# Optimization experiments

Measured on AMD Instinct MI355X. Metric: run time of the kernel, lower is better.

Reference implementation:

```python
import jax, jax.numpy as jnp
import numpy as np

B, N, K, OUT = 8, 2048, 20, 40
BN_EPS = 1e-5  # torch BatchNorm default eps; inference with running_mean=0, running_var=1


def knn_idx(x, k):
    # x: (B, C, N). distance[b,n,m] = -||x_n||^2 - ||x_m||^2 + 2 x_n.x_m (negative sq dist)
    xsqu = jnp.sum(x * x, axis=1, keepdims=True)              # (B,1,N)
    xx = jnp.einsum('bcn,bcm->bnm', x, x)                     # (B,N,N)
    dist = 2.0 * xx - xsqu - jnp.transpose(xsqu, (0, 2, 1))   # (B,N,N)
    _, idx = jax.lax.top_k(dist, k)                           # (B,N,k) nearest (incl. self)
    return idx


def get_graph_feature(x, k):
    # x: (B, C, N) -> edge features (B, N, k, 2C) = concat(nbr - ctr, ctr)
    Bb = x.shape[0]
    idx = knn_idx(x, k)
    xt = jnp.transpose(x, (0, 2, 1))                          # (B,N,C)
    nbr = xt[jnp.arange(Bb)[:, None, None], idx]              # (B,N,k,C) gather
    ctr = xt[:, :, None, :]
    return jnp.concatenate([nbr - ctr, jnp.broadcast_to(ctr, nbr.shape)], axis=-1)


def bn(h, g, b):
    # inference BatchNorm with running_mean=0, running_var=1 (affine only)
    return h * (g / jnp.sqrt(1.0 + BN_EPS)) + b


def edge_conv(x, w, g, b, k):
    # EdgeConv: knn -> gather edge feats -> 1x1 conv -> BN -> ReLU -> max over k
    feat = get_graph_feature(x, k)                            # (B,N,k,2C)
    h = jnp.einsum('bnkc,oc->bnko', feat, w)                  # 1x1 conv
    h = jax.nn.relu(bn(h, g, b))
    h = jnp.max(h, axis=2)                                    # max pool over k -> (B,N,O)
    return jnp.transpose(h, (0, 2, 1))                        # (B,O,N)


def _forward(x, conv_w1, conv_w2, conv_w3, conv_w4, conv_w5, fc_w1, fc_w2, fc_w3,
             bn_g1, bn_b1, bn_g2, bn_b2, bn_g3, bn_b3, bn_g4, bn_b4,
             bn_g5, bn_b5, bn_g6, bn_b6, bn_g7, bn_b7, k):
    x1 = edge_conv(x, conv_w1, bn_g1, bn_b1, k)               # (B,64,N)
    x2 = edge_conv(x1, conv_w2, bn_g2, bn_b2, k)              # (B,64,N)
    x3 = edge_conv(x2, conv_w3, bn_g3, bn_b3, k)              # (B,128,N)
    x4 = edge_conv(x3, conv_w4, bn_g4, bn_b4, k)              # (B,256,N)
    xc = jnp.concatenate([x1, x2, x3, x4], axis=1)            # (B,512,N)
    h = jnp.einsum('bcn,oc->bon', xc, conv_w5)                # (B,1024,N)
    h = jax.nn.relu(bn(h, bn_g5[:, None], bn_b5[:, None]))
    h = jnp.max(h, axis=-1)                                   # global max pool -> (B,1024)
    h = jax.nn.relu(bn(h @ fc_w1.T, bn_g6, bn_b6))            # dropout = identity (eval)
    h = jax.nn.relu(bn(h @ fc_w2.T, bn_g7, bn_b7))
    return h @ fc_w3.T                                        # (B,OUT)


def setup_inputs() -> dict:
    key = jax.random.key(0)
    ks = jax.random.split(key, 32)
    def w(i, shape):
        return jax.random.normal(ks[i], shape, jnp.float32) / np.sqrt(shape[-1]).astype(np.float32)
    inp = {
        'x': jax.random.normal(ks[0], (B, 3, N), jnp.float32),
        'conv_w1': w(1, (64, 6)),
        'conv_w2': w(2, (64, 128)),
        'conv_w3': w(3, (128, 128)),
        'conv_w4': w(4, (256, 256)),
        'conv_w5': w(5, (1024, 512)),
        'fc_w1': w(6, (512, 1024)),
        'fc_w2': w(7, (256, 512)),
        'fc_w3': w(8, (OUT, 256)),
    }
    dims = [64, 64, 128, 256, 1024, 512, 256]
    for i, d in enumerate(dims):
        inp['bn_g%d' % (i + 1)] = jax.random.uniform(ks[9 + i], (d,), jnp.float32, 0.5, 1.5)
        inp['bn_b%d' % (i + 1)] = 0.05 * jax.random.normal(ks[16 + i], (d,), jnp.float32)
    inp['k'] = K
    return inp


def reference(x, conv_w1, conv_w2, conv_w3, conv_w4, conv_w5, fc_w1, fc_w2, fc_w3,
              bn_g1, bn_b1, bn_g2, bn_b2, bn_g3, bn_b3, bn_g4, bn_b4,
              bn_g5, bn_b5, bn_g6, bn_b6, bn_g7, bn_b7, k):
    return _forward(x, conv_w1, conv_w2, conv_w3, conv_w4, conv_w5, fc_w1, fc_w2, fc_w3,
                    bn_g1, bn_b1, bn_g2, bn_b2, bn_g3, bn_b3, bn_g4, bn_b4,
                    bn_g5, bn_b5, bn_g6, bn_b6, bn_g7, bn_b7, k)
```

## Files before the change

### kernel.cpp

```cpp
#include <hip/hip_runtime.h>
#include <hip/hip_bf16.h>
#include <math.h>

#define BATCH 8
#define NPTS  2048
#define KNN   20
#define NEG_INF (-3.402823466e38f)

static __device__ __forceinline__ float bn_scale(float g){ return g * rsqrtf(1.0f + 1e-5f); }

static __device__ __forceinline__ unsigned short bf16r(float f){
  unsigned int u = __float_as_uint(f);
  unsigned int r = (u + 0x7fffu + ((u >> 16) & 1u)) >> 16;
  return (unsigned short)r;
}
static __device__ __forceinline__ float bf2f(unsigned short h){
  return __uint_as_float((unsigned int)h << 16);
}
static __device__ __forceinline__ unsigned int fenc(float f){
  unsigned int u = __float_as_uint(f);
  return (u & 0x80000000u) ? ~u : (u | 0x80000000u);
}
static __device__ __forceinline__ float fdec(unsigned int e){
  return __uint_as_float((e & 0x80000000u) ? (e & 0x7fffffffu) : ~e);
}

using bfrag = __attribute__((ext_vector_type(8))) short;
using f32x4 = __attribute__((ext_vector_type(4))) float;

template<int CTRL>
static __device__ __forceinline__ void dpp_amax(float &bv, int &bi){
  int ov_i = __builtin_amdgcn_update_dpp(__float_as_int(NEG_INF), __float_as_int(bv),
                                         CTRL, 0xf, 0xf, false);
  int oi   = __builtin_amdgcn_update_dpp(0x7fffffff, bi, CTRL, 0xf, 0xf, false);
  float ov = __int_as_float(ov_i);
  if (ov > bv || (ov == bv && oi < bi)){ bv = ov; bi = oi; }
}
static __device__ __forceinline__ int wave_argmax_idx(float bv, int bi){
  dpp_amax<0x111>(bv, bi);
  dpp_amax<0x112>(bv, bi);
  dpp_amax<0x114>(bv, bi);
  dpp_amax<0x118>(bv, bi);
  dpp_amax<0x142>(bv, bi);
  dpp_amax<0x143>(bv, bi);
  return __builtin_amdgcn_readlane(bi, 63);
}
template<int CTRL>
static __device__ __forceinline__ float dpp_fadd(float v){
  int ov = __builtin_amdgcn_update_dpp(0, __float_as_int(v), CTRL, 0xf, 0xf, false);
  return v + __int_as_float(ov);
}
static __device__ __forceinline__ float wave_sum(float v){
  v = dpp_fadd<0x111>(v); v = dpp_fadd<0x112>(v);
  v = dpp_fadd<0x114>(v); v = dpp_fadd<0x118>(v);
  v = dpp_fadd<0x142>(v); v = dpp_fadd<0x143>(v);
  return __int_as_float(__builtin_amdgcn_readlane(__float_as_int(v), 63));
}

__global__ void sqnorm_kernel(const float* __restrict__ X, float* __restrict__ sq, int C){
  int i = blockIdx.x*blockDim.x + threadIdx.x;
  if (i >= BATCH*NPTS) return;
  int b = i / NPTS, n = i - b*NPTS;
  const float* xb = X + (size_t)b*C*NPTS + n;
  float s = 0.f;
  for (int c=0;c<C;++c){ float v = xb[(size_t)c*NPTS]; s += v*v; }
  sq[i] = s;
}

template<int C>
__global__ __launch_bounds__(256, 2) void knn_kernel(const float* __restrict__ X,
                                                     const float* __restrict__ sq,
                                                     int* __restrict__ idxout){
  const int b = blockIdx.y;
  const int n0 = blockIdx.x * 8;
  const int t = threadIdx.x;
  __shared__ __align__(16) float dist[4][NPTS];
  __shared__ float ctrs[C][8];
  __shared__ float sqn[8];
  const float* xb = X + (size_t)b*C*NPTS;
  for (int i=t; i<C*8; i+=256){
    int c = i >> 3, p = i & 7;
    ctrs[c][p] = xb[(size_t)c*NPTS + n0 + p];
  }
  if (t < 8) sqn[t] = sq[b*NPTS + n0 + t];
  __syncthreads();

  const int m0 = t * 8;
  float acc[8][8];
  #pragma unroll
  for (int i=0;i<8;++i)
    #pragma unroll
    for (int j=0;j<8;++j) acc[i][j] = 0.f;
  for (int c=0;c<C;++c){
    const float4 xa = *(const float4*)&xb[(size_t)c*NPTS + m0];
    const float4 xc = *(const float4*)&xb[(size_t)c*NPTS + m0 + 4];
    const float xm[8] = {xa.x,xa.y,xa.z,xa.w,xc.x,xc.y,xc.z,xc.w};
    #pragma unroll
    for (int i=0;i<8;++i){
      const float cv = ctrs[c][i];
      #pragma unroll
      for (int j=0;j<8;++j) acc[i][j] += cv*xm[j];
    }
  }
  {
    const float4 sa = *(const float4*)&sq[b*NPTS + m0];
    const float4 sb = *(const float4*)&sq[b*NPTS + m0 + 4];
    const float sm[8] = {sa.x,sa.y,sa.z,sa.w,sb.x,sb.y,sb.z,sb.w};
    #pragma unroll
    for (int i=0;i<8;++i){
      const float si = sqn[i];
      #pragma unroll
      for (int j=0;j<8;++j) acc[i][j] = 2.f*acc[i][j] - si - sm[j];
    }
  }

  const int wv = t >> 6, lane = t & 63;
  #pragma unroll
  for (int rep=0; rep<2; ++rep){
    #pragma unroll
    for (int i=0;i<4;++i){
      *(float4*)&dist[i][m0]   = make_float4(acc[rep*4+i][0],acc[rep*4+i][1],acc[rep*4+i][2],acc[rep*4+i][3]);
      *(float4*)&dist[i][m0+4] = make_float4(acc[rep*4+i][4],acc[rep*4+i][5],acc[rep*4+i][6],acc[rep*4+i][7]);
    }
    __syncthreads();
    float s0=NEG_INF,s1=NEG_INF,s2=NEG_INF,s3=NEG_INF;
    int   i0=0x7fffffff,i1=0x7fffffff,i2=0x7fffffff,i3=0x7fffffff;
    #pragma unroll
    for (int j=0;j<32;++j){
      const float v = dist[wv][lane + 64*j];
      const int   m = lane + 64*j;
      const bool b0 = v > s0, b1 = v > s1, b2 = v > s2, b3 = v > s3;
      const float n0 = b0 ? v : s0;            const int q0 = b0 ? m : i0;
      const float n1 = b0 ? s0 : (b1 ? v : s1); const int q1 = b0 ? i0 : (b1 ? m : i1);
      const float n2 = b1 ? s1 : (b2 ? v : s2); const int q2 = b1 ? i1 : (b2 ? m : i2);
      const float n3 = b2 ? s2 : (b3 ? v : s3); const int q3 = b2 ? i2 : (b3 ? m : i3);
      s0=n0;s1=n1;s2=n2;s3=n3; i0=q0;i1=q1;i2=q2;i3=q3;
    }
    int rem = 4;
    int* row = idxout + ((size_t)b*NPTS + n0 + rep*4 + wv)*KNN;
    for (int sel=0; sel<KNN; ++sel){
      const int widx = wave_argmax_idx(s0, i0);
      if (lane == 0) row[sel] = widx;
      if ((widx & 63) == lane){
        const float lastv = s0; const int lasti = i0;
        s0=s1;i0=i1; s1=s2;i1=i2; s2=s3;i2=i3;
        rem--;
        if (rem == 0){
          float nv = NEG_INF; int ni = 0x7fffffff;
          #pragma unroll
          for (int j=0;j<32;++j){
            const float vv = dist[wv][lane + 64*j];
            const int   mi = lane + 64*j;
            const bool ok = (vv < lastv) || (vv == lastv && mi > lasti);
            if (ok && vv > nv){ nv = vv; ni = mi; }
          }
          s0 = nv; i0 = ni; rem = 1;
        }
      }
    }
    __syncthreads();
  }
}

__global__ void wprep_kernel(const float* __restrict__ w, float* __restrict__ wnT,
                             float* __restrict__ wdT, int O, int C){
  int i = blockIdx.x*blockDim.x + threadIdx.x;
  if (i >= O*C) return;
  int c = i / O, o = i - c*O;
  float a = w[(size_t)o*2*C + c];
  wnT[(size_t)c*O + o] = a;
  wdT[(size_t)c*O + o] = w[(size_t)o*2*C + C + c] - a;
}

__global__ void wprep_bf_kernel(const float* __restrict__ w, unsigned short* __restrict__ wn,
                                unsigned short* __restrict__ wd, int O, int C){
  int i = blockIdx.x*blockDim.x + threadIdx.x;
  if (i >= O*C) return;
  int o = i / C, c = i - o*C;
  float a = w[(size_t)o*2*C + c];
  float d = w[(size_t)o*2*C + C + c] - a;
  wn[(size_t)o*C + c] = bf16r(a);
  wd[(size_t)o*C + c] = bf16r(d);
}

__global__ void bfsplit_kernel(const float* __restrict__ in, unsigned short* __restrict__ hi,
                               unsigned short* __restrict__ lo, int nq){
  int i = blockIdx.x*blockDim.x + threadIdx.x;
  if (i >= nq) return;
  float4 v = *(const float4*)&in[(size_t)i*4];
  unsigned short h0=bf16r(v.x), h1=bf16r(v.y), h2=bf16r(v.z), h3=bf16r(v.w);
  unsigned short l0=bf16r(v.x-bf2f(h0)), l1=bf16r(v.y-bf2f(h1)),
                 l2=bf16r(v.z-bf2f(h2)), l3=bf16r(v.w-bf2f(h3));
  *(uint2*)&hi[(size_t)i*4] = make_uint2((unsigned)h0|((unsigned)h1<<16), (unsigned)h2|((unsigned)h3<<16));
  *(uint2*)&lo[(size_t)i*4] = make_uint2((unsigned)l0|((unsigned)l1<<16), (unsigned)l2|((unsigned)l3<<16));
}

__global__ __launch_bounds__(256) void xcat_kernel(const float* __restrict__ x1T,
    const float* __restrict__ x2T, const float* __restrict__ x3T, const float* __restrict__ x4T,
    unsigned short* __restrict__ xhi, unsigned short* __restrict__ xlo){
  int i = blockIdx.x*blockDim.x + threadIdx.x;
  if (i >= BATCH*NPTS*128) return;
  int q = i & 127, bn_ = i >> 7;
  int k = q*4;
  const float* src; int kk;
  if (k < 64)      { src = x1T + (size_t)bn_*64;  kk = k; }
  else if (k <128) { src = x2T + (size_t)bn_*64;  kk = k-64; }
  else if (k <256) { src = x3T + (size_t)bn_*128; kk = k-128; }
  else             { src = x4T + (size_t)bn_*256; kk = k-256; }
  float4 v = *(const float4*)&src[kk];
  unsigned short h0=bf16r(v.x), h1=bf16r(v.y), h2=bf16r(v.z), h3=bf16r(v.w);
  unsigned short l0=bf16r(v.x-bf2f(h0)), l1=bf16r(v.y-bf2f(h1)),
                 l2=bf16r(v.z-bf2f(h2)), l3=bf16r(v.w-bf2f(h3));
  *(uint2*)&xhi[(size_t)i*4] = make_uint2((unsigned)h0|((unsigned)h1<<16), (unsigned)h2|((unsigned)h3<<16));
  *(uint2*)&xlo[(size_t)i*4] = make_uint2((unsigned)l0|((unsigned)l1<<16), (unsigned)l2|((unsigned)l3<<16));
}

__global__ __launch_bounds__(256) void transpose2d_kernel(const float* __restrict__ in,
    float* __restrict__ out, int R, int Cc){
  __shared__ float tile[32][33];
  const size_t boff = (size_t)blockIdx.z * (size_t)R * Cc;
  const int c0 = blockIdx.x*32, r0 = blockIdx.y*32;
  const int tx = threadIdx.x & 31, ty = threadIdx.x >> 5;
  #pragma unroll
  for (int j=0;j<4;++j){
    int r = ty*4 + j;
    tile[r][tx] = in[boff + (size_t)(r0+r)*Cc + c0 + tx];
  }
  __syncthreads();
  #pragma unroll
  for (int j=0;j<4;++j){
    int r = ty*4 + j;
    out[boff + (size_t)(c0+r)*R + r0 + tx] = tile[tx][r];
  }
}

__global__ void xt0_kernel(const float* __restrict__ x, float* __restrict__ xT0){
  int i = blockIdx.x*blockDim.x + threadIdx.x;
  if (i >= BATCH*NPTS) return;
  int b = i / NPTS, n = i - b*NPTS;
  const float* xb = x + (size_t)b*3*NPTS;
  float v0 = xb[n], v1 = xb[NPTS + n], v2 = xb[2*NPTS + n];
  float* o = xT0 + ((size_t)b*NPTS + n)*3;
  o[0]=v0; o[1]=v1; o[2]=v2;
}

__global__ __launch_bounds__(256) void edgeconv1_kernel(const float* __restrict__ xT0,
    const int* __restrict__ idx, const float* __restrict__ wnT, const float* __restrict__ wdT,
    const float* __restrict__ g, const float* __restrict__ bb, float* __restrict__ outT){
  const int b = blockIdx.y, n0 = blockIdx.x*4, t = threadIdx.x;
  __shared__ float nbr[4][KNN][3];
  __shared__ float ctr[4][3];
  __shared__ int   idxs[4][KNN];
  const float* xb = xT0 + (size_t)b*NPTS*3;
  if (t < 4*KNN) idxs[t/KNN][t%KNN] = idx[((size_t)b*NPTS + n0 + t/KNN)*KNN + (t%KNN)];
  if (t >= 128 && t < 140){ int i = t-128; ctr[i/3][i%3] = xb[(size_t)(n0 + i/3)*3 + i%3]; }
  __syncthreads();
  for (int i=t; i<4*KNN*3; i+=256){
    int p = i/(KNN*3), r = i - p*(KNN*3), k = r/3, c = r - k*3;
    nbr[p][k][c] = xb[(size_t)idxs[p][k]*3 + c];
  }
  __syncthreads();
  const int p = t >> 6, o = t & 63;
  const float wn0 = wnT[o], wn1 = wnT[64+o], wn2 = wnT[128+o];
  const float cst = ctr[p][0]*wdT[o] + ctr[p][1]*wdT[64+o] + ctr[p][2]*wdT[128+o];
  float best = NEG_INF;
  #pragma unroll
  for (int k=0;k<KNN;++k){
    float a = nbr[p][k][0]*wn0 + nbr[p][k][1]*wn1 + nbr[p][k][2]*wn2;
    best = fmaxf(best, a);
  }
  float vv = (best + cst) * bn_scale(g[o]) + bb[o];
  outT[((size_t)b*NPTS + n0 + p)*64 + o] = fmaxf(vv, 0.f);
}

template<int C, int O>
__global__ __launch_bounds__(256) void edgeconv_mfma(const float* __restrict__ xT,
    const int* __restrict__ idx,
    const unsigned short* __restrict__ wn_bf, const unsigned short* __restrict__ wd_bf,
    const float* __restrict__ g, const float* __restrict__ bb, float* __restrict__ outT){
  constexpr int ROWS = 112;
  constexpr int CP   = C + 8;
  constexpr int KS   = C / 32;
  constexpr int NTW  = O / 64;
  __shared__ __align__(16) unsigned short A[ROWS][CP];
  __shared__ unsigned int res[4][O];
  __shared__ float cst_s[4][O];
  __shared__ int idxs[4][KNN];
  const int b = blockIdx.y, n0 = blockIdx.x*4, t = threadIdx.x;
  const float* xTb = xT + (size_t)b*NPTS*C;
  if (t < 4*KNN) idxs[t/KNN][t%KNN] = idx[((size_t)b*NPTS + n0 + t/KNN)*KNN + (t%KNN)];
  for (int i=t; i<4*O; i+=256) res[i/O][i & (O-1)] = 0u;
  __syncthreads();
  for (int i=t; i<ROWS*(C/4); i+=256){
    int r = i/(C/4), c4 = i - r*(C/4);
    float4 v = make_float4(0.f,0.f,0.f,0.f);
    if (r < 96){
      int p = r/24, kk = r - p*24;
      int src = idxs[p][kk < KNN ? kk : 0];
      v = *(const float4*)&xTb[(size_t)src*C + c4*4];
    } else if (r < 100){
      v = *(const float4*)&xTb[(size_t)(n0 + (r-96))*C + c4*4];
    }
    unsigned int lo = (unsigned int)bf16r(v.x) | ((unsigned int)bf16r(v.y) << 16);
    unsigned int hi = (unsigned int)bf16r(v.z) | ((unsigned int)bf16r(v.w) << 16);
    *(uint2*)&A[r][c4*4] = make_uint2(lo, hi);
  }
  __syncthreads();

  const int wv = t >> 6, l = t & 63;
  const int lane15 = l & 15, quad = l >> 4;
  bfrag Bn[NTW][KS];
  #pragma unroll
  for (int nt=0; nt<NTW; ++nt){
    const int col = (wv*NTW + nt)*16 + lane15;
    #pragma unroll
    for (int s=0; s<KS; ++s)
      Bn[nt][s] = *(const bfrag*)&wn_bf[(size_t)col*C + s*32 + quad*8];
  }
  #pragma unroll
  for (int mt=0; mt<7; ++mt){
    bfrag Af[KS];
    #pragma unroll
    for (int s=0; s<KS; ++s)
      Af[s] = *(const bfrag*)&A[mt*16 + lane15][s*32 + quad*8];
    if (mt < 6){
      const int rbase = mt*16 + quad*4;
      const int p = rbase / 24;
      #pragma unroll
      for (int nt=0; nt<NTW; ++nt){
        f32x4 acc = {0.f,0.f,0.f,0.f};
        #pragma unroll
        for (int s=0; s<KS; ++s)
          acc = __builtin_amdgcn_mfma_f32_16x16x32_bf16(Af[s], Bn[nt][s], acc, 0, 0, 0);
        float m = fmaxf(fmaxf(acc[0], acc[1]), fmaxf(acc[2], acc[3]));
        const int col = (wv*NTW + nt)*16 + lane15;
        atomicMax(&res[p][col], fenc(m));
      }
    } else {
      #pragma unroll
      for (int nt=0; nt<NTW; ++nt){
        const int col = (wv*NTW + nt)*16 + lane15;
        f32x4 acc = {0.f,0.f,0.f,0.f};
        #pragma unroll
        for (int s=0; s<KS; ++s){
          bfrag Bd = *(const bfrag*)&wd_bf[(size_t)col*C + s*32 + quad*8];
          acc = __builtin_amdgcn_mfma_f32_16x16x32_bf16(Af[s], Bd, acc, 0, 0, 0);
        }
        if (quad == 0){
          #pragma unroll
          for (int r=0;r<4;++r) cst_s[r][col] = acc[r];
        }
      }
    }
  }
  __syncthreads();
  for (int i=t; i<4*O; i+=256){
    int p = i/O, o = i - p*O;
    float mx = fdec(res[p][o]);
    float vv = (mx + cst_s[p][o]) * bn_scale(g[o]) + bb[o];
    outT[((size_t)b*NPTS + n0 + p)*O + o] = fmaxf(vv, 0.f);
  }
}

__global__ __launch_bounds__(256) void conv5_v3(const unsigned short* __restrict__ xhi,
    const unsigned short* __restrict__ xlo, const unsigned short* __restrict__ whi,
    const unsigned short* __restrict__ wlo, const float* __restrict__ g,
    const float* __restrict__ bb, float* __restrict__ out5){
  __shared__ __align__(16) unsigned short Ah_s[128*32];
  __shared__ __align__(16) unsigned short Al_s[128*32];
  __shared__ __align__(16) unsigned short Bh_s[64*32];
  __shared__ __align__(16) unsigned short Bl_s[64*32];
  const int t = threadIdx.x;
  const int row0 = blockIdx.x*128, o0 = blockIdx.y*64;
  const int b = row0 / NPTS;
  const int wv = t >> 6, l = t & 63, lane15 = l & 15, quad = l >> 4;
  const int ar = t >> 2, ac = (t & 3)*8;
  const unsigned short* gAh0 = xhi + (size_t)(row0 + ar)*512 + ac;
  const unsigned short* gAh1 = xhi + (size_t)(row0 + 64 + ar)*512 + ac;
  const unsigned short* gAl0 = xlo + (size_t)(row0 + ar)*512 + ac;
  const unsigned short* gAl1 = xlo + (size_t)(row0 + 64 + ar)*512 + ac;
  const unsigned short* gBh  = whi + (size_t)(o0 + ar)*512 + ac;
  const unsigned short* gBl  = wlo + (size_t)(o0 + ar)*512 + ac;

  uint4 pf0 = *(const uint4*)gAh0;
  uint4 pf1 = *(const uint4*)gAh1;
  uint4 pf2 = *(const uint4*)gAl0;
  uint4 pf3 = *(const uint4*)gAl1;
  uint4 pf4 = *(const uint4*)gBh;
  uint4 pf5 = *(const uint4*)gBl;

  f32x4 acc[2][4];
  #pragma unroll
  for (int mt=0;mt<2;++mt)
    #pragma unroll
    for (int nt=0;nt<4;++nt) acc[mt][nt] = (f32x4){0.f,0.f,0.f,0.f};

  for (int ks=0; ks<16; ++ks){
    *(uint4*)&Ah_s[t*8]        = pf0;
    *(uint4*)&Ah_s[2048 + t*8] = pf1;
    *(uint4*)&Al_s[t*8]        = pf2;
    *(uint4*)&Al_s[2048 + t*8] = pf3;
    *(uint4*)&Bh_s[t*8]        = pf4;
    *(uint4*)&Bl_s[t*8]        = pf5;
    __syncthreads();
    if (ks < 15){
      const int koff = (ks+1)*32;
      pf0 = *(const uint4*)(gAh0 + koff);
      pf1 = *(const uint4*)(gAh1 + koff);
      pf2 = *(const uint4*)(gAl0 + koff);
      pf3 = *(const uint4*)(gAl1 + koff);
      pf4 = *(const uint4*)(gBh  + koff);
      pf5 = *(const uint4*)(gBl  + koff);
    }
    bfrag Afh[2], Afl[2], Bfh[4], Bfl[4];
    #pragma unroll
    for (int mt=0;mt<2;++mt){
      const int m = wv*32 + mt*16 + lane15;
      Afh[mt] = *(const bfrag*)&Ah_s[m*32 + quad*8];
      Afl[mt] = *(const bfrag*)&Al_s[m*32 + quad*8];
    }
    #pragma unroll
    for (int nt=0;nt<4;++nt){
      const int oc = nt*16 + lane15;
      Bfh[nt] = *(const bfrag*)&Bh_s[oc*32 + quad*8];
      Bfl[nt] = *(const bfrag*)&Bl_s[oc*32 + quad*8];
    }
    #pragma unroll
    for (int mt=0;mt<2;++mt)
      #pragma unroll
      for (int nt=0;nt<4;++nt){
        acc[mt][nt] = __builtin_amdgcn_mfma_f32_16x16x32_bf16(Afh[mt], Bfh[nt], acc[mt][nt], 0, 0, 0);
        acc[mt][nt] = __builtin_amdgcn_mfma_f32_16x16x32_bf16(Afl[mt], Bfh[nt], acc[mt][nt], 0, 0, 0);
        acc[mt][nt] = __builtin_amdgcn_mfma_f32_16x16x32_bf16(Afh[mt], Bfl[nt], acc[mt][nt], 0, 0, 0);
      }
    __syncthreads();
  }
  #pragma unroll
  for (int nt=0;nt<4;++nt){
    float m = NEG_INF;
    #pragma unroll
    for (int mt=0;mt<2;++mt)
      #pragma unroll
      for (int r=0;r<4;++r) m = fmaxf(m, acc[mt][nt][r]);
    m = fmaxf(m, __shfl_xor(m, 16, 64));
    m = fmaxf(m, __shfl_xor(m, 32, 64));
    if (quad == 0){
      const int o = o0 + nt*16 + lane15;
      float vv = fmaxf(m * bn_scale(g[o]) + bb[o], 0.f);
      atomicMax((int*)&out5[(size_t)b*1024 + o], __float_as_int(vv));
    }
  }
}

__global__ void zero_kernel(float* __restrict__ p, int nfloats){
  int i = blockIdx.x*blockDim.x + threadIdx.x;
  if (i < nfloats) p[i] = 0.f;
}

__global__ __launch_bounds__(256) void fc_wave_kernel(const float* __restrict__ in,
    const float* __restrict__ w, const float* __restrict__ g, const float* __restrict__ bb,
    float* __restrict__ out, int IN, int O){
  const int wid = (blockIdx.x*256 + threadIdx.x) >> 6;
  const int lane = threadIdx.x & 63;
  if (wid >= BATCH*O) return;
  const int b = wid / O, o = wid - b*O;
  const float* inb = in + (size_t)b*IN;
  const float* wo  = w + (size_t)o*IN;
  float s = 0.f;
  for (int c = lane; c < IN; c += 64) s += inb[c]*wo[c];
  s = wave_sum(s);
  if (lane == 0){
    if (g){ s = s*bn_scale(g[o]) + bb[o]; s = fmaxf(s, 0.f); }
    out[wid] = s;
  }
}

extern "C" void kernel_launch(void* const* d_in, const int* in_sizes, int n_in,
                              void* d_out, int out_size, void* d_ws, size_t ws_size,
                              hipStream_t stream){
  const float* x   = (const float*)d_in[0];
  const float* w1  = (const float*)d_in[1];
  const float* w2  = (const float*)d_in[2];
  const float* w3  = (const float*)d_in[3];
  const float* w4  = (const float*)d_in[4];
  const float* w5  = (const float*)d_in[5];
  const float* fw1 = (const float*)d_in[6];
  const float* fw2 = (const float*)d_in[7];
  const float* fw3 = (const float*)d_in[8];
  const float* g1 = (const float*)d_in[9];  const float* b1 = (const float*)d_in[10];
  const float* g2 = (const float*)d_in[11]; const float* b2 = (const float*)d_in[12];
  const float* g3 = (const float*)d_in[13]; const float* b3 = (const float*)d_in[14];
  const float* g4 = (const float*)d_in[15]; const float* b4 = (const float*)d_in[16];
  const float* g5 = (const float*)d_in[17]; const float* b5 = (const float*)d_in[18];
  const float* g6 = (const float*)d_in[19]; const float* b6 = (const float*)d_in[20];
  const float* g7 = (const float*)d_in[21]; const float* b7 = (const float*)d_in[22];

  float* ws = (float*)d_ws;
  size_t off = 0;
  float* x1  = ws + off; off += (size_t)BATCH*64*NPTS;
  float* x2  = ws + off; off += (size_t)BATCH*64*NPTS;
  float* x3  = ws + off; off += (size_t)BATCH*128*NPTS;
  unsigned short* xcat_lo = (unsigned short*)x1;
  unsigned short* xcat_hi = (unsigned short*)(ws + off); off += (size_t)BATCH*256*NPTS;
  float* x1T = ws + off; off += (size_t)BATCH*64*NPTS;
  float* x2T = ws + off; off += (size_t)BATCH*64*NPTS;
  float* x3T = ws + off; off += (size_t)BATCH*128*NPTS;
  float* x4T = ws + off; off += (size_t)BATCH*256*NPTS;
  float* xT0 = ws + off; off += (size_t)BATCH*3*NPTS;
  float* sq  = ws + off; off += (size_t)BATCH*NPTS;
  int*  idx  = (int*)(ws + off); off += (size_t)BATCH*NPTS*KNN;
  float* out5 = ws + off; off += BATCH*1024;
  float* h6 = ws + off;   off += BATCH*512;
  float* h7 = ws + off;   off += BATCH*256;
  float* wnT1 = ws + off; off += 3*64;
  float* wdT1 = ws + off; off += 3*64;
  unsigned short* wn2 = (unsigned short*)(ws + off); off += 64*64/2;
  unsigned short* wd2 = (unsigned short*)(ws + off); off += 64*64/2;
  unsigned short* wn3 = (unsigned short*)(ws + off); off += 128*64/2;
  unsigned short* wd3 = (unsigned short*)(ws + off); off += 128*64/2;
  unsigned short* wn4 = (unsigned short*)(ws + off); off += 256*128/2;
  unsigned short* wd4 = (unsigned short*)(ws + off); off += 256*128/2;
  unsigned short* w5hi = (unsigned short*)(ws + off); off += 1024*512/2;
  unsigned short* w5lo = (unsigned short*)(ws + off); off += 1024*512/2;

  dim3 gridKNN(NPTS/8, BATCH);
  dim3 gridEC(NPTS/4, BATCH);

  xt0_kernel<<<64, 256, 0, stream>>>(x, xT0);
  sqnorm_kernel<<<64, 256, 0, stream>>>(x, sq, 3);
  knn_kernel<3><<<gridKNN, 256, 0, stream>>>(x, sq, idx);
  wprep_kernel<<<1, 256, 0, stream>>>(w1, wnT1, wdT1, 64, 3);
  edgeconv1_kernel<<<gridEC, 256, 0, stream>>>(xT0, idx, wnT1, wdT1, g1, b1, x1T);
  transpose2d_kernel<<<dim3(2,64,BATCH), 256, 0, stream>>>(x1T, x1, NPTS, 64);
  sqnorm_kernel<<<64, 256, 0, stream>>>(x1, sq, 64);
  knn_kernel<64><<<gridKNN, 256, 0, stream>>>(x1, sq, idx);
  wprep_bf_kernel<<<16, 256, 0, stream>>>(w2, wn2, wd2, 64, 64);
  edgeconv_mfma<64,64><<<gridEC, 256, 0, stream>>>(x1T, idx, wn2, wd2, g2, b2, x2T);
  transpose2d_kernel<<<dim3(2,64,BATCH), 256, 0, stream>>>(x2T, x2, NPTS, 64);
  sqnorm_kernel<<<64, 256, 0, stream>>>(x2, sq, 64);
  knn_kernel<64><<<gridKNN, 256, 0, stream>>>(x2, sq, idx);
  wprep_bf_kernel<<<32, 256, 0, stream>>>(w3, wn3, wd3, 128, 64);
  edgeconv_mfma<64,128><<<gridEC, 256, 0, stream>>>(x2T, idx, wn3, wd3, g3, b3, x3T);
  transpose2d_kernel<<<dim3(4,64,BATCH), 256, 0, stream>>>(x3T, x3, NPTS, 128);
  sqnorm_kernel<<<64, 256, 0, stream>>>(x3, sq, 128);
  knn_kernel<128><<<gridKNN, 256, 0, stream>>>(x3, sq, idx);
  wprep_bf_kernel<<<128, 256, 0, stream>>>(w4, wn4, wd4, 256, 128);
  edgeconv_mfma<128,256><<<gridEC, 256, 0, stream>>>(x3T, idx, wn4, wd4, g4, b4, x4T);
  xcat_kernel<<<(BATCH*NPTS*128)/256, 256, 0, stream>>>(x1T, x2T, x3T, x4T, xcat_hi, xcat_lo);
  bfsplit_kernel<<<512, 256, 0, stream>>>(w5, w5hi, w5lo, 1024*512/4);
  zero_kernel<<<32, 256, 0, stream>>>(out5, BATCH*1024);
  conv5_v3<<<dim3(BATCH*NPTS/128, 16), 256, 0, stream>>>(xcat_hi, xcat_lo, w5hi, w5lo, g5, b5, out5);
  fc_wave_kernel<<<(BATCH*512*64)/256, 256, 0, stream>>>(out5, fw1, g6, b6, h6, 1024, 512);
  fc_wave_kernel<<<(BATCH*256*64)/256, 256, 0, stream>>>(h6, fw2, g7, b7, h7, 512, 256);
  fc_wave_kernel<<<(BATCH*40*64 + 255)/256, 256, 0, stream>>>(h7, fw3, nullptr, nullptr, (float*)d_out, 256, 40);
}
```

Baseline: 867.6 us.

## Replace fp32 knn for layers 2-4 with split-bf16 MFMA distance GEMM plus selection

For layers 2-4 the fused fp32 knn kernel is replaced by a split-bf16 (hi/lo, three-product) MFMA GEMM that writes a full per-batch N×N distance matrix to a global scratch buffer. A separate selection kernel then reads each row with float4 loads and does the top-20 selection. The point-major features are split into the concatenated hi/lo bf16 buffer as each layer finishes, which removes the transpose kernels and the final xcat pass. The cost is a 16 MB distance write and read per batch, run as 8 sequential batch launches per layer, and distances that carry bf16-split precision error that could change neighbour order on ties.

```diff
diff --git a/kernel.cpp b/kernel.cpp
--- a/kernel.cpp
+++ b/kernel.cpp
@@ -27,6 +27,7 @@
 
 using bfrag = __attribute__((ext_vector_type(8))) short;
 using f32x4 = __attribute__((ext_vector_type(4))) float;
+using f32x2 = __attribute__((ext_vector_type(2))) float;
 
 template<int CTRL>
 static __device__ __forceinline__ void dpp_amax(float &bv, int &bi){
@@ -56,6 +57,15 @@
   v = dpp_fadd<0x142>(v); v = dpp_fadd<0x143>(v);
   return __int_as_float(__builtin_amdgcn_readlane(__float_as_int(v), 63));
 }
+static __device__ __forceinline__ void ins4(float v, int m,
+    float&s0,float&s1,float&s2,float&s3,int&i0,int&i1,int&i2,int&i3){
+  const bool b0 = v > s0, b1 = v > s1, b2 = v > s2, b3 = v > s3;
+  const float n0 = b0 ? v : s0;             const int q0 = b0 ? m : i0;
+  const float n1 = b0 ? s0 : (b1 ? v : s1); const int q1 = b0 ? i0 : (b1 ? m : i1);
+  const float n2 = b1 ? s1 : (b2 ? v : s2); const int q2 = b1 ? i1 : (b2 ? m : i2);
+  const float n3 = b2 ? s2 : (b3 ? v : s3); const int q3 = b2 ? i2 : (b3 ? m : i3);
+  s0=n0;s1=n1;s2=n2;s3=n3; i0=q0;i1=q1;i2=q2;i3=q3;
+}
 
 __global__ void sqnorm_kernel(const float* __restrict__ X, float* __restrict__ sq, int C){
   int i = blockIdx.x*blockDim.x + threadIdx.x;
@@ -64,6 +74,18 @@
   const float* xb = X + (size_t)b*C*NPTS + n;
   float s = 0.f;
   for (int c=0;c<C;++c){ float v = xb[(size_t)c*NPTS]; s += v*v; }
+  sq[i] = s;
+}
+
+__global__ void sqnorm_pm_kernel(const float* __restrict__ xT, float* __restrict__ sq, int C){
+  int i = blockIdx.x*blockDim.x + threadIdx.x;
+  if (i >= BATCH*NPTS) return;
+  const float* r = xT + (size_t)i*C;
+  float s = 0.f;
+  for (int c4=0; c4<C; c4+=4){
+    float4 v = *(const float4*)&r[c4];
+    s += v.x*v.x; s += v.y*v.y; s += v.z*v.z; s += v.w*v.w;
+  }
   sq[i] = s;
 }
 
@@ -128,13 +150,7 @@
     #pragma unroll
     for (int j=0;j<32;++j){
       const float v = dist[wv][lane + 64*j];
-      const int   m = lane + 64*j;
-      const bool b0 = v > s0, b1 = v > s1, b2 = v > s2, b3 = v > s3;
-      const float n0 = b0 ? v : s0;            const int q0 = b0 ? m : i0;
-      const float n1 = b0 ? s0 : (b1 ? v : s1); const int q1 = b0 ? i0 : (b1 ? m : i1);
-      const float n2 = b1 ? s1 : (b2 ? v : s2); const int q2 = b1 ? i1 : (b2 ? m : i2);
-      const float n3 = b2 ? s2 : (b3 ? v : s3); const int q3 = b2 ? i2 : (b3 ? m : i3);
-      s0=n0;s1=n1;s2=n2;s3=n3; i0=q0;i1=q1;i2=q2;i3=q3;
+      ins4(v, lane + 64*j, s0,s1,s2,s3, i0,i1,i2,i3);
     }
     int rem = 4;
     int* row = idxout + ((size_t)b*NPTS + n0 + rep*4 + wv)*KNN;
@@ -162,6 +178,127 @@
   }
 }
 
+template<int CK>
+__global__ __launch_bounds__(256) void distgemm(const unsigned short* __restrict__ xh,
+    const unsigned short* __restrict__ xl, const float* __restrict__ sqb,
+    float* __restrict__ D){
+  constexpr int KSTEPS = CK/32;
+  __shared__ __align__(16) unsigned short Ah_s[128*32];
+  __shared__ __align__(16) unsigned short Al_s[128*32];
+  __shared__ __align__(16) unsigned short Bh_s[64*32];
+  __shared__ __align__(16) unsigned short Bl_s[64*32];
+  const int t = threadIdx.x;
+  const int n0 = blockIdx.x*128, m0 = blockIdx.y*64;
+  const int wv = t >> 6, l = t & 63, lane15 = l & 15, quad = l >> 4;
+  const int ar = t >> 2, ac = (t & 3)*8;
+  f32x4 acc[2][4];
+  #pragma unroll
+  for (int mt=0;mt<2;++mt)
+    #pragma unroll
+    for (int nt=0;nt<4;++nt) acc[mt][nt] = (f32x4){0.f,0.f,0.f,0.f};
+
+  for (int ks=0; ks<KSTEPS; ++ks){
+    const int ko = ks*32 + ac;
+    uint4 a0 = *(const uint4*)&xh[(size_t)(n0 + ar)*512 + ko];
+    uint4 a1 = *(const uint4*)&xh[(size_t)(n0 + 64 + ar)*512 + ko];
+    uint4 a2 = *(const uint4*)&xl[(size_t)(n0 + ar)*512 + ko];
+    uint4 a3 = *(const uint4*)&xl[(size_t)(n0 + 64 + ar)*512 + ko];
+    uint4 bh = *(const uint4*)&xh[(size_t)(m0 + ar)*512 + ko];
+    uint4 bl = *(const uint4*)&xl[(size_t)(m0 + ar)*512 + ko];
+    *(uint4*)&Ah_s[t*8]        = a0;
+    *(uint4*)&Ah_s[2048 + t*8] = a1;
+    *(uint4*)&Al_s[t*8]        = a2;
+    *(uint4*)&Al_s[2048 + t*8] = a3;
+    *(uint4*)&Bh_s[t*8]        = bh;
+    *(uint4*)&Bl_s[t*8]        = bl;
+    __syncthreads();
+    bfrag Afh[2], Afl[2], Bfh[4], Bfl[4];
+    #pragma unroll
+    for (int mt=0;mt<2;++mt){
+      const int r = wv*32 + mt*16 + lane15;
+      Afh[mt] = *(const bfrag*)&Ah_s[r*32 + quad*8];
+      Afl[mt] = *(const bfrag*)&Al_s[r*32 + quad*8];
+    }
+    #pragma unroll
+    for (int nt=0;nt<4;++nt){
+      const int c = nt*16 + lane15;
+      Bfh[nt] = *(const bfrag*)&Bh_s[c*32 + quad*8];
+      Bfl[nt] = *(const bfrag*)&Bl_s[c*32 + quad*8];
+    }
+    #pragma unroll
+    for (int mt=0;mt<2;++mt)
+      #pragma unroll
+      for (int nt=0;nt<4;++nt){
+        acc[mt][nt] = __builtin_amdgcn_mfma_f32_16x16x32_bf16(Afh[mt], Bfh[nt], acc[mt][nt], 0, 0, 0);
+        acc[mt][nt] = __builtin_amdgcn_mfma_f32_16x16x32_bf16(Afh[mt], Bfl[nt], acc[mt][nt], 0, 0, 0);
+        acc[mt][nt] = __builtin_amdgcn_mfma_f32_16x16x32_bf16(Afl[mt], Bfh[nt], acc[mt][nt], 0, 0, 0);
+      }
+    __syncthreads();
+  }
+  float sqn_r[2][4];
+  #pragma unroll
+  for (int mt=0;mt<2;++mt)
+    #pragma unroll
+    for (int r=0;r<4;++r) sqn_r[mt][r] = sqb[n0 + wv*32 + mt*16 + quad*4 + r];
+  #pragma unroll
+  for (int nt=0;nt<4;++nt){
+    const int m = m0 + nt*16 + lane15;
+    const float sqm = sqb[m];
+    #pragma unroll
+    for (int mt=0;mt<2;++mt)
+      #pragma unroll
+      for (int r=0;r<4;++r){
+        const int n = n0 + wv*32 + mt*16 + quad*4 + r;
+        D[(size_t)n*NPTS + m] = 2.f*acc[mt][nt][r] - sqn_r[mt][r] - sqm;
+      }
+  }
+}
+
+__global__ __launch_bounds__(256) void knn_select(const float* __restrict__ D,
+                                                  int* __restrict__ idxb){
+  const int p = blockIdx.x*4 + (threadIdx.x >> 6);
+  const int lane = threadIdx.x & 63;
+  const float4* row4 = (const float4*)(D + (size_t)p*NPTS);
+  float s0=NEG_INF,s1=NEG_INF,s2=NEG_INF,s3=NEG_INF;
+  int   i0=0x7fffffff,i1=0x7fffffff,i2=0x7fffffff,i3=0x7fffffff;
+  #pragma unroll
+  for (int j=0;j<8;++j){
+    const float4 v4 = row4[lane + 64*j];
+    const int mb = (lane + 64*j)*4;
+    ins4(v4.x, mb+0, s0,s1,s2,s3, i0,i1,i2,i3);
+    ins4(v4.y, mb+1, s0,s1,s2,s3, i0,i1,i2,i3);
+    ins4(v4.z, mb+2, s0,s1,s2,s3, i0,i1,i2,i3);
+    ins4(v4.w, mb+3, s0,s1,s2,s3, i0,i1,i2,i3);
+  }
+  int rem = 4;
+  int* out = idxb + p*KNN;
+  for (int sel=0; sel<KNN; ++sel){
+    const int widx = wave_argmax_idx(s0, i0);
+    if (lane == 0) out[sel] = widx;
+    if (((widx >> 2) & 63) == lane){
+      const float lastv = s0; const int lasti = i0;
+      s0=s1;i0=i1; s1=s2;i1=i2; s2=s3;i2=i3;
+      rem--;
+      if (rem == 0){
+        float nv = NEG_INF; int ni = 0x7fffffff;
+        #pragma unroll
+        for (int j=0;j<8;++j){
+          const float4 v4 = row4[lane + 64*j];
+          const int mb = (lane + 64*j)*4;
+          const float va[4] = {v4.x, v4.y, v4.z, v4.w};
+          #pragma unroll
+          for (int e=0;e<4;++e){
+            const float vv = va[e]; const int mi = mb + e;
+            const bool ok = (vv < lastv) || (vv == lastv && mi > lasti);
+            if (ok && vv > nv){ nv = vv; ni = mi; }
+          }
+        }
+        s0 = nv; i0 = ni; rem = 1;
+      }
+    }
+  }
+}
+
 __global__ void wprep_kernel(const float* __restrict__ w, float* __restrict__ wnT,
                              float* __restrict__ wdT, int O, int C){
   int i = blockIdx.x*blockDim.x + threadIdx.x;
@@ -195,43 +332,18 @@
   *(uint2*)&lo[(size_t)i*4] = make_uint2((unsigned)l0|((unsigned)l1<<16), (unsigned)l2|((unsigned)l3<<16));
 }
 
-__global__ __launch_bounds__(256) void xcat_kernel(const float* __restrict__ x1T,
-    const float* __restrict__ x2T, const float* __restrict__ x3T, const float* __restrict__ x4T,
-    unsigned short* __restrict__ xhi, unsigned short* __restrict__ xlo){
-  int i = blockIdx.x*blockDim.x + threadIdx.x;
-  if (i >= BATCH*NPTS*128) return;
-  int q = i & 127, bn_ = i >> 7;
-  int k = q*4;
-  const float* src; int kk;
-  if (k < 64)      { src = x1T + (size_t)bn_*64;  kk = k; }
-  else if (k <128) { src = x2T + (size_t)bn_*64;  kk = k-64; }
-  else if (k <256) { src = x3T + (size_t)bn_*128; kk = k-128; }
-  else             { src = x4T + (size_t)bn_*256; kk = k-256; }
-  float4 v = *(const float4*)&src[kk];
+__global__ __launch_bounds__(256) void xsplit_kernel(const float* __restrict__ src,
+    unsigned short* __restrict__ hi, unsigned short* __restrict__ lo, int Cq){
+  int i = blockIdx.x*blockDim.x + threadIdx.x;
+  if (i >= BATCH*NPTS*Cq) return;
+  int bn_ = i / Cq, q = i - bn_*Cq;
+  float4 v = *(const float4*)&src[(size_t)i*4];
   unsigned short h0=bf16r(v.x), h1=bf16r(v.y), h2=bf16r(v.z), h3=bf16r(v.w);
   unsigned short l0=bf16r(v.x-bf2f(h0)), l1=bf16r(v.y-bf2f(h1)),
                  l2=bf16r(v.z-bf2f(h2)), l3=bf16r(v.w-bf2f(h3));
-  *(uint2*)&xhi[(size_t)i*4] = make_uint2((unsigned)h0|((unsigned)h1<<16), (unsigned)h2|((unsigned)h3<<16));
-  *(uint2*)&xlo[(size_t)i*4] = make_uint2((unsigned)l0|((unsigned)l1<<16), (unsigned)l2|((unsigned)l3<<16));
-}
-
-__global__ __launch_bounds__(256) void transpose2d_kernel(const float* __restrict__ in,
-    float* __restrict__ out, int R, int Cc){
-  __shared__ float tile[32][33];
-  const size_t boff = (size_t)blockIdx.z * (size_t)R * Cc;
-  const int c0 = blockIdx.x*32, r0 = blockIdx.y*32;
-  const int tx = threadIdx.x & 31, ty = threadIdx.x >> 5;
-  #pragma unroll
-  for (int j=0;j<4;++j){
-    int r = ty*4 + j;
-    tile[r][tx] = in[boff + (size_t)(r0+r)*Cc + c0 + tx];
-  }
-  __syncthreads();
-  #pragma unroll
-  for (int j=0;j<4;++j){
-    int r = ty*4 + j;
-    out[boff + (size_t)(c0+r)*R + r0 + tx] = tile[tx][r];
-  }
+  const size_t d = (size_t)bn_*512 + q*4;
+  *(uint2*)&hi[d] = make_uint2((unsigned)h0|((unsigned)h1<<16), (unsigned)h2|((unsigned)h3<<16));
+  *(uint2*)&lo[d] = make_uint2((unsigned)l0|((unsigned)l1<<16), (unsigned)l2|((unsigned)l3<<16));
 }
 
 __global__ void xt0_kernel(const float* __restrict__ x, float* __restrict__ xT0){
@@ -497,15 +609,13 @@
 
   float* ws = (float*)d_ws;
   size_t off = 0;
-  float* x1  = ws + off; off += (size_t)BATCH*64*NPTS;
-  float* x2  = ws + off; off += (size_t)BATCH*64*NPTS;
-  float* x3  = ws + off; off += (size_t)BATCH*128*NPTS;
-  unsigned short* xcat_lo = (unsigned short*)x1;
   unsigned short* xcat_hi = (unsigned short*)(ws + off); off += (size_t)BATCH*256*NPTS;
+  unsigned short* xcat_lo = (unsigned short*)(ws + off); off += (size_t)BATCH*256*NPTS;
   float* x1T = ws + off; off += (size_t)BATCH*64*NPTS;
   float* x2T = ws + off; off += (size_t)BATCH*64*NPTS;
   float* x3T = ws + off; off += (size_t)BATCH*128*NPTS;
   float* x4T = ws + off; off += (size_t)BATCH*256*NPTS;
+  float* Dbuf = x4T;
   float* xT0 = ws + off; off += (size_t)BATCH*3*NPTS;
   float* sq  = ws + off; off += (size_t)BATCH*NPTS;
   int*  idx  = (int*)(ws + off); off += (size_t)BATCH*NPTS*KNN;
@@ -525,28 +635,44 @@
 
   dim3 gridKNN(NPTS/8, BATCH);
   dim3 gridEC(NPTS/4, BATCH);
+  dim3 gridDG(NPTS/128, NPTS/64);
 
   xt0_kernel<<<64, 256, 0, stream>>>(x, xT0);
   sqnorm_kernel<<<64, 256, 0, stream>>>(x, sq, 3);
   knn_kernel<3><<<gridKNN, 256, 0, stream>>>(x, sq, idx);
   wprep_kernel<<<1, 256, 0, stream>>>(w1, wnT1, wdT1, 64, 3);
   edgeconv1_kernel<<<gridEC, 256, 0, stream>>>(xT0, idx, wnT1, wdT1, g1, b1, x1T);
-  transpose2d_kernel<<<dim3(2,64,BATCH), 256, 0, stream>>>(x1T, x1, NPTS, 64);
-  sqnorm_kernel<<<64, 256, 0, stream>>>(x1, sq, 64);
-  knn_kernel<64><<<gridKNN, 256, 0, stream>>>(x1, sq, idx);
+  xsplit_kernel<<<(BATCH*NPTS*16)/256, 256, 0, stream>>>(x1T, xcat_hi, xcat_lo, 16);
+  sqnorm_pm_kernel<<<64, 256, 0, stream>>>(x1T, sq, 64);
+  for (int b=0; b<BATCH; ++b){
+    distgemm<64><<<gridDG, 256, 0, stream>>>(xcat_hi + (size_t)b*NPTS*512,
+                                             xcat_lo + (size_t)b*NPTS*512,
+                                             sq + (size_t)b*NPTS, Dbuf);
+    knn_select<<<NPTS/4, 256, 0, stream>>>(Dbuf, idx + (size_t)b*NPTS*KNN);
+  }
   wprep_bf_kernel<<<16, 256, 0, stream>>>(w2, wn2, wd2, 64, 64);
   edgeconv_mfma<64,64><<<gridEC, 256, 0, stream>>>(x1T, idx, wn2, wd2, g2, b2, x2T);
-  transpose2d_kernel<<<dim3(2,64,BATCH), 256, 0, stream>>>(x2T, x2, NPTS, 64);
-  sqnorm_kernel<<<64, 256, 0, stream>>>(x2, sq, 64);
-  knn_kernel<64><<<gridKNN, 256, 0, stream>>>(x2, sq, idx);
+  xsplit_kernel<<<(BATCH*NPTS*16)/256, 256, 0, stream>>>(x2T, xcat_hi + 64, xcat_lo + 64, 16);
+  sqnorm_pm_kernel<<<64, 256, 0, stream>>>(x2T, sq, 64);
+  for (int b=0; b<BATCH; ++b){
+    distgemm<64><<<gridDG, 256, 0, stream>>>(xcat_hi + (size_t)b*NPTS*512 + 64,
+                                             xcat_lo + (size_t)b*NPTS*512 + 64,
+                                             sq + (size_t)b*NPTS, Dbuf);
+    knn_select<<<NPTS/4, 256, 0, stream>>>(Dbuf, idx + (size_t)b*NPTS*KNN);
+  }
   wprep_bf_kernel<<<32, 256, 0, stream>>>(w3, wn3, wd3, 128, 64);
   edgeconv_mfma<64,128><<<gridEC, 256, 0, stream>>>(x2T, idx, wn3, wd3, g3, b3, x3T);
-  transpose2d_kernel<<<dim3(4,64,BATCH), 256, 0, stream>>>(x3T, x3, NPTS, 128);
-  sqnorm_kernel<<<64, 256, 0, stream>>>(x3, sq, 128);
-  knn_kernel<128><<<gridKNN, 256, 0, stream>>>(x3, sq, idx);
+  xsplit_kernel<<<(BATCH*NPTS*32)/256, 256, 0, stream>>>(x3T, xcat_hi + 128, xcat_lo + 128, 32);
+  sqnorm_pm_kernel<<<64, 256, 0, stream>>>(x3T, sq, 128);
+  for (int b=0; b<BATCH; ++b){
+    distgemm<128><<<gridDG, 256, 0, stream>>>(xcat_hi + (size_t)b*NPTS*512 + 128,
+                                              xcat_lo + (size_t)b*NPTS*512 + 128,
+                                              sq + (size_t)b*NPTS, Dbuf);
+    knn_select<<<NPTS/4, 256, 0, stream>>>(Dbuf, idx + (size_t)b*NPTS*KNN);
+  }
   wprep_bf_kernel<<<128, 256, 0, stream>>>(w4, wn4, wd4, 256, 128);
   edgeconv_mfma<128,256><<<gridEC, 256, 0, stream>>>(x3T, idx, wn4, wd4, g4, b4, x4T);
-  xcat_kernel<<<(BATCH*NPTS*128)/256, 256, 0, stream>>>(x1T, x2T, x3T, x4T, xcat_hi, xcat_lo);
+  xsplit_kernel<<<(BATCH*NPTS*64)/256, 256, 0, stream>>>(x4T, xcat_hi + 256, xcat_lo + 256, 64);
   bfsplit_kernel<<<512, 256, 0, stream>>>(w5, w5hi, w5lo, 1024*512/4);
   zero_kernel<<<32, 256, 0, stream>>>(out5, BATCH*1024);
   conv5_v3<<<dim3(BATCH*NPTS/128, 16), 256, 0, stream>>>(xcat_hi, xcat_lo, w5hi, w5lo, g5, b5, out5);
```

Result: slower. 1.067 ms (+23.0%).
